# Performance work log

Measured on AMD Instinct MI355X. Metric: run time of the kernel, lower is better.

Reference implementation:

```python
import jax, jax.numpy as jnp
import numpy as np

B, S, I, C, P = 64, 14, 32, 10, 4   # batch, spatial, in-caps/pos, classes, pose size
ROUTINGS = 3
EPS = 1e-9


def setup_inputs() -> dict:
    key = jax.random.key(0)
    k1, k2, k3, k4, k5 = jax.random.split(key, 5)
    return {
        "inputs_pose": jax.random.normal(k1, (B, S, S, I, P, P), jnp.float32),
        "inputs_activation": jax.random.uniform(k2, (B, S, S, I), jnp.float32),
        "w": jax.random.normal(k3, (1, I, C, P, P), jnp.float32),
        "beta_v": jax.random.normal(k4, (1, C), jnp.float32) * 0.1,
        "beta_a": jax.random.normal(k5, (1, C), jnp.float32) * 0.1,
    }


def _em_routing(votes, i_act, beta_v, beta_a, routings):
    # votes: [B, N, C, 16], i_act: [B, N]
    Bn, N, Cc, D = votes.shape
    rr = jnp.full((Bn, N, Cc, 1), 1.0 / Cc, votes.dtype)  # uniform init assignments
    bv = beta_v.reshape(1, 1, Cc, 1)
    ba = beta_a.reshape(1, 1, Cc, 1)
    it_min, it_max = 1.0, min(float(routings), 3.0)  # inverse-temperature schedule
    o_mean = o_act = None
    for it in range(routings):
        inv_temp = it_min + (it_max - it_min) * it / max(1.0, routings - 1.0)
        # --- M step ---
        rr_p = rr * i_act[:, :, None, None]                        # [B,N,C,1]
        rr_sum = jnp.sum(rr_p, axis=1, keepdims=True)              # [B,1,C,1]
        o_mean = jnp.sum(rr_p * votes, axis=1, keepdims=True) / rr_sum   # [B,1,C,16]
        o_var = jnp.sum(rr_p * jnp.square(votes - o_mean), axis=1, keepdims=True) / rr_sum
        o_stdv = jnp.sqrt(o_var)                                   # [B,1,C,16]
        cost = jnp.sum((bv + jnp.log(o_stdv + EPS)) * rr_sum, axis=-1, keepdims=True)  # [B,1,C,1]
        o_act = jax.nn.sigmoid(inv_temp * (ba - cost))             # [B,1,C,1]
        # --- E step (skipped on last iteration) ---
        if it < routings - 1:
            logp = (-jnp.sum(jnp.square(votes - o_mean) / (2.0 * jnp.square(o_stdv) + EPS),
                             axis=-1, keepdims=True)
                    - jnp.sum(jnp.log(o_stdv + EPS), axis=-1, keepdims=True))  # [B,N,C,1]
            zz = jnp.log(o_act + EPS) + logp
            rr = jax.nn.softmax(zz, axis=2)
    return o_mean[:, 0], o_act[:, 0, :, 0]  # [B,C,16], [B,C]


def reference(inputs_pose, inputs_activation, w, beta_v, beta_a):
    # mat_transform: votes[b,h,w,i,c] = pose[b,h,w,i] @ W[i,c]   (4x4 matmuls)
    votes = jnp.einsum('bhwipq,icqr->bhwicpr', inputs_pose, w[0])
    votes = votes.reshape(B, S, S, I, C, P * P)
    # coordinate addition: scaled (row+0.5)/S onto pose element 0, col onto element 1
    coord = (jnp.arange(S, dtype=votes.dtype) + 0.5) / S
    votes = votes.at[..., 0].add(coord[None, :, None, None, None])
    votes = votes.at[..., 1].add(coord[None, None, :, None, None])
    votes = votes.reshape(B, S * S * I, C, P * P)
    acts = inputs_activation.reshape(B, S * S * I)
    o_mean, o_act = _em_routing(votes, acts, beta_v, beta_a, ROUTINGS)
    pose = o_mean.reshape(B, C, P, P)
    return pose, o_act
```

## Files before the change

### kernel.cpp

```cpp
#include <hip/hip_runtime.h>
#include <math.h>

#define Bsz 64
#define Ssz 14
#define Isz 32
#define Csz 10
#define Dsz 16
#define Nsz (Ssz*Ssz*Isz)
#define EPSF 1e-9f

#define CH  640
#define NCH 10

__device__ __forceinline__ void load_pose(const float* __restrict__ poseb, int n, float* p)
{
    const float4* pp = reinterpret_cast<const float4*>(poseb + (size_t)n * Dsz);
    float4 a0 = pp[0], a1 = pp[1], a2 = pp[2], a3 = pp[3];
    p[0]=a0.x; p[1]=a0.y; p[2]=a0.z; p[3]=a0.w;
    p[4]=a1.x; p[5]=a1.y; p[6]=a1.z; p[7]=a1.w;
    p[8]=a2.x; p[9]=a2.y; p[10]=a2.z; p[11]=a2.w;
    p[12]=a3.x; p[13]=a3.y; p[14]=a3.z; p[15]=a3.w;
}

__device__ __forceinline__ void vote_reg(const float* p, const float* Wr,
                                         float chh, float cww, float* v)
{
#pragma unroll
    for (int pr = 0; pr < 4; ++pr)
#pragma unroll
        for (int r = 0; r < 4; ++r)
            v[pr*4+r] = p[pr*4+0]*Wr[0*4+r] + p[pr*4+1]*Wr[1*4+r]
                      + p[pr*4+2]*Wr[2*4+r] + p[pr*4+3]*Wr[3*4+r];
    v[0] += chh;
    v[1] += cww;
}

__device__ __forceinline__ void load_W_regs(const float* __restrict__ w,
                                            int lane, int c, float* Wr)
{
    const float4* ws = reinterpret_cast<const float4*>(w + (((lane & 31)*Csz + c) * Dsz));
    float4 b0 = ws[0], b1 = ws[1], b2 = ws[2], b3 = ws[3];
    Wr[0]=b0.x; Wr[1]=b0.y; Wr[2]=b0.z; Wr[3]=b0.w;
    Wr[4]=b1.x; Wr[5]=b1.y; Wr[6]=b1.z; Wr[7]=b1.w;
    Wr[8]=b2.x; Wr[9]=b2.y; Wr[10]=b2.z; Wr[11]=b2.w;
    Wr[12]=b3.x; Wr[13]=b3.y; Wr[14]=b3.z; Wr[15]=b3.w;
}

__global__ __launch_bounds__(640) void m0_kernel(
    const float* __restrict__ pose,
    const float* __restrict__ act,
    const float* __restrict__ w,
    float* __restrict__ partials)
{
    const int b = blockIdx.x, chunk = blockIdx.y;
    const int tid = threadIdx.x, c = tid >> 6, lane = tid & 63;

    float Wr[16];
    load_W_regs(w, lane, c, Wr);

    float s0 = 0.f, s1[Dsz], s2[Dsz];
#pragma unroll
    for (int d = 0; d < Dsz; ++d) { s1[d] = 0.f; s2[d] = 0.f; }

    const float* poseb = pose + (size_t)b * Nsz * Dsz;
    const float* actb  = act  + (size_t)b * Nsz;
    const int base = chunk * CH;

    for (int nl = lane; nl < CH; nl += 64) {
        const int n = base + nl;
        if (n < Nsz) {
            float p[16];
            load_pose(poseb, n, p);
            int hw = n >> 5;
            int wc = hw % Ssz, hr = hw / Ssz;
            float wgt = actb[n] * (1.0f/Csz);
            float v[16];
            vote_reg(p, Wr, (hr+0.5f)*(1.0f/Ssz), (wc+0.5f)*(1.0f/Ssz), v);
            s0 += wgt;
#pragma unroll
            for (int d = 0; d < Dsz; ++d) {
                float wv = wgt * v[d];
                s1[d] += wv;
                s2[d] += wv * v[d];
            }
        }
    }

#pragma unroll
    for (int m = 32; m >= 1; m >>= 1) {
        s0 += __shfl_xor(s0, m);
#pragma unroll
        for (int d = 0; d < Dsz; ++d) {
            s1[d] += __shfl_xor(s1[d], m);
            s2[d] += __shfl_xor(s2[d], m);
        }
    }
    if (lane == 0) {
        float* pt = partials + ((size_t)(b*Csz + c)*NCH + chunk)*33;
        pt[0] = s0;
#pragma unroll
        for (int d = 0; d < Dsz; ++d) { pt[1+d] = s1[d]; pt[17+d] = s2[d]; }
    }
}

__global__ __launch_bounds__(640) void em_kernel(
    const float* __restrict__ pose,
    const float* __restrict__ act,
    const float* __restrict__ w,
    const float* __restrict__ beta_v,
    const float* __restrict__ beta_a,
    const float* __restrict__ part_in,
    float* __restrict__ part_out,
    float inv_temp_prev)
{
    const int b = blockIdx.x, chunk = blockIdx.y;
    const int tid = threadIdx.x, wv = tid >> 6, lane = tid & 63;

    __shared__ float zz[CH][11];
    __shared__ float Sv[Csz][33];
    __shared__ float prm[Csz][33];
    __shared__ float lg[Csz][16];

    float Wr[16];
    load_W_regs(w, lane, wv, Wr);

    if (tid < Csz*33) {
        int c = tid / 33, j = tid - c*33;
        const float* pp = part_in + ((size_t)(b*Csz + c)*NCH)*33 + j;
        float s = 0.f;
        for (int ch2 = 0; ch2 < NCH; ++ch2) s += pp[ch2*33];
        Sv[c][j] = s;
    }
    __syncthreads();
    if (tid < Csz*Dsz) {
        int c = tid >> 4, d = tid & 15;
        float S0 = Sv[c][0];
        float mn  = Sv[c][1+d] / S0;
        float var = fmaxf(Sv[c][17+d] / S0 - mn*mn, 0.f);
        prm[c][d]    = mn;
        prm[c][16+d] = 1.f / (2.f*var + EPSF);
        lg[c][d]     = __logf(sqrtf(var) + EPSF);
    }
    __syncthreads();
    if (tid < Csz) {
        int c = tid;
        float sumlog = 0.f;
#pragma unroll
        for (int d = 0; d < Dsz; ++d) sumlog += lg[c][d];
        float cost = Sv[c][0] * (16.f * beta_v[c] + sumlog);
        float oact = 1.f / (1.f + __expf(-inv_temp_prev * (beta_a[c] - cost)));
        prm[c][32] = __logf(oact + EPSF) - sumlog;
    }
    __syncthreads();

    const int base = chunk * CH;
    const float* poseb = pose + (size_t)b * Nsz * Dsz;

    {
        float mn[Dsz], iv[Dsz];
#pragma unroll
        for (int d = 0; d < Dsz; ++d) { mn[d] = prm[wv][d]; iv[d] = prm[wv][16+d]; }
        float Kc = prm[wv][32];

        for (int nl = lane; nl < CH; nl += 64) {
            const int n = base + nl;
            if (n < Nsz) {
                float p[16];
                load_pose(poseb, n, p);
                int hw = n >> 5;
                int wc = hw % Ssz, hr = hw / Ssz;
                float v[16];
                vote_reg(p, Wr, (hr+0.5f)*(1.0f/Ssz), (wc+0.5f)*(1.0f/Ssz), v);
                float quad = 0.f;
#pragma unroll
                for (int d = 0; d < Dsz; ++d) {
                    float dv = v[d] - mn[d];
                    quad += dv * dv * iv[d];
                }
                zz[nl][wv] = Kc - quad;
            }
        }
    }
    __syncthreads();

    {
        const int n = base + tid;
        if (n < Nsz) {
            float z[Csz];
#pragma unroll
            for (int c = 0; c < Csz; ++c) z[c] = zz[tid][c];
            float zmax = z[0];
#pragma unroll
            for (int c = 1; c < Csz; ++c) zmax = fmaxf(zmax, z[c]);
            float zsum = 0.f;
#pragma unroll
            for (int c = 0; c < Csz; ++c) { z[c] = __expf(z[c] - zmax); zsum += z[c]; }
            float sc = __fdividef(act[(size_t)b*Nsz + n], zsum);
#pragma unroll
            for (int c = 0; c < Csz; ++c) zz[tid][c] = z[c] * sc;
        }
    }
    __syncthreads();

    float s0 = 0.f, s1[Dsz], s2[Dsz];
#pragma unroll
    for (int d = 0; d < Dsz; ++d) { s1[d] = 0.f; s2[d] = 0.f; }

    for (int nl = lane; nl < CH; nl += 64) {
        const int n = base + nl;
        if (n < Nsz) {
            float p[16];
            load_pose(poseb, n, p);
            int hw = n >> 5;
            int wc = hw % Ssz, hr = hw / Ssz;
            float wgt = zz[nl][wv];
            float v[16];
            vote_reg(p, Wr, (hr+0.5f)*(1.0f/Ssz), (wc+0.5f)*(1.0f/Ssz), v);
            s0 += wgt;
#pragma unroll
            for (int d = 0; d < Dsz; ++d) {
                float wvv = wgt * v[d];
                s1[d] += wvv;
                s2[d] += wvv * v[d];
            }
        }
    }

#pragma unroll
    for (int m = 32; m >= 1; m >>= 1) {
        s0 += __shfl_xor(s0, m);
#pragma unroll
        for (int d = 0; d < Dsz; ++d) {
            s1[d] += __shfl_xor(s1[d], m);
            s2[d] += __shfl_xor(s2[d], m);
        }
    }
    if (lane == 0) {
        float* pt = part_out + ((size_t)(b*Csz + wv)*NCH + chunk)*33;
        pt[0] = s0;
#pragma unroll
        for (int d = 0; d < Dsz; ++d) { pt[1+d] = s1[d]; pt[17+d] = s2[d]; }
    }
}

__global__ __launch_bounds__(64) void fin_kernel(
    const float* __restrict__ partials,
    const float* __restrict__ beta_v,
    const float* __restrict__ beta_a,
    float* __restrict__ out,
    float inv_temp)
{
    const int bc = blockIdx.x * 64 + threadIdx.x;
    if (bc >= Bsz*Csz) return;
    const int c = bc % Csz;

    float S[33];
#pragma unroll
    for (int j = 0; j < 33; ++j) S[j] = 0.f;
    const float* pb = partials + (size_t)bc * NCH * 33;
    for (int ch2 = 0; ch2 < NCH; ++ch2)
#pragma unroll
        for (int j = 0; j < 33; ++j) S[j] += pb[ch2*33 + j];

    float S0 = S[0], rS0 = 1.f / S0;
    float sumlog = 0.f;
    float* om = out + (size_t)bc * Dsz;
#pragma unroll
    for (int d = 0; d < Dsz; ++d) {
        float mn  = S[1+d] * rS0;
        float var = fmaxf(S[17+d] * rS0 - mn*mn, 0.f);
        sumlog += __logf(sqrtf(var) + EPSF);
        om[d] = mn;
    }
    float cost = S0 * (16.f * beta_v[c] + sumlog);
    float oact = 1.f / (1.f + __expf(-inv_temp * (beta_a[c] - cost)));
    out[Bsz*Csz*Dsz + bc] = oact;
}

extern "C" void kernel_launch(void* const* d_in, const int* in_sizes, int n_in,
                              void* d_out, int out_size, void* d_ws, size_t ws_size,
                              hipStream_t stream)
{
    const float* pose = (const float*)d_in[0];
    const float* act  = (const float*)d_in[1];
    const float* w    = (const float*)d_in[2];
    const float* bv   = (const float*)d_in[3];
    const float* ba   = (const float*)d_in[4];
    float* out = (float*)d_out;

    float* partA = (float*)d_ws;
    float* partB = partA + (size_t)Bsz*Csz*NCH*33;

    dim3 grid(Bsz, NCH);

    m0_kernel<<<grid, CH, 0, stream>>>(pose, act, w, partA);
    em_kernel<<<grid, CH, 0, stream>>>(pose, act, w, bv, ba, partA, partB, 1.0f);
    em_kernel<<<grid, CH, 0, stream>>>(pose, act, w, bv, ba, partB, partA, 2.0f);
    fin_kernel<<<(Bsz*Csz + 63)/64, 64, 0, stream>>>(partA, bv, ba, out, 3.0f);
}
```

Baseline: 233.2 us.

## Stage pose chunk in LDS and rechunk N into exact 448-element tiles

Each block now copies its chunk of pose matrices into shared memory once, cooperatively with float4 loads. The ten class wavefronts then read that chunk from LDS instead of each re-reading it from global memory. The chunk size changes from 640 to 448 so that the 6272 inputs split evenly into 14 chunks; this removes the bounds checks and the partially empty last chunk, while the block stays at 640 threads. The cost is about 28 KB more shared memory per block, which may reduce occupancy, and the 64-byte per-lane stride of the LDS reads can cause bank conflicts.

```diff
diff --git a/kernel.cpp b/kernel.cpp
--- a/kernel.cpp
+++ b/kernel.cpp
@@ -9,18 +9,10 @@
 #define Nsz (Ssz*Ssz*Isz)
 #define EPSF 1e-9f
 
-#define CH  640
-#define NCH 10
-
-__device__ __forceinline__ void load_pose(const float* __restrict__ poseb, int n, float* p)
-{
-    const float4* pp = reinterpret_cast<const float4*>(poseb + (size_t)n * Dsz);
-    float4 a0 = pp[0], a1 = pp[1], a2 = pp[2], a3 = pp[3];
-    p[0]=a0.x; p[1]=a0.y; p[2]=a0.z; p[3]=a0.w;
-    p[4]=a1.x; p[5]=a1.y; p[6]=a1.z; p[7]=a1.w;
-    p[8]=a2.x; p[9]=a2.y; p[10]=a2.z; p[11]=a2.w;
-    p[12]=a3.x; p[13]=a3.y; p[14]=a3.z; p[15]=a3.w;
-}
+#define CH   448
+#define NCH  14
+#define BLK  640
+#define ITER (CH/64)
 
 __device__ __forceinline__ void vote_reg(const float* p, const float* Wr,
                                          float chh, float cww, float* v)
@@ -46,7 +38,17 @@
     Wr[12]=b3.x; Wr[13]=b3.y; Wr[14]=b3.z; Wr[15]=b3.w;
 }
 
-__global__ __launch_bounds__(640) void m0_kernel(
+__device__ __forceinline__ void load_pose_lds(const float* Pl, int nl, float* p)
+{
+    const float4* pp = reinterpret_cast<const float4*>(Pl + nl*Dsz);
+    float4 a0 = pp[0], a1 = pp[1], a2 = pp[2], a3 = pp[3];
+    p[0]=a0.x; p[1]=a0.y; p[2]=a0.z; p[3]=a0.w;
+    p[4]=a1.x; p[5]=a1.y; p[6]=a1.z; p[7]=a1.w;
+    p[8]=a2.x; p[9]=a2.y; p[10]=a2.z; p[11]=a2.w;
+    p[12]=a3.x; p[13]=a3.y; p[14]=a3.z; p[15]=a3.w;
+}
+
+__global__ __launch_bounds__(BLK) void m0_kernel(
     const float* __restrict__ pose,
     const float* __restrict__ act,
     const float* __restrict__ w,
@@ -54,35 +56,43 @@
 {
     const int b = blockIdx.x, chunk = blockIdx.y;
     const int tid = threadIdx.x, c = tid >> 6, lane = tid & 63;
+    const int base = chunk * CH;
+
+    __shared__ float Pl[CH*Dsz];
+
+    const float* poseb = pose + (size_t)b * Nsz * Dsz;
+    {
+        const float4* gp = reinterpret_cast<const float4*>(poseb + (size_t)base * Dsz);
+        float4* lp = reinterpret_cast<float4*>(Pl);
+        for (int t = tid; t < CH*4; t += BLK) lp[t] = gp[t];
+    }
 
     float Wr[16];
     load_W_regs(w, lane, c, Wr);
+    __syncthreads();
 
     float s0 = 0.f, s1[Dsz], s2[Dsz];
 #pragma unroll
     for (int d = 0; d < Dsz; ++d) { s1[d] = 0.f; s2[d] = 0.f; }
 
-    const float* poseb = pose + (size_t)b * Nsz * Dsz;
-    const float* actb  = act  + (size_t)b * Nsz;
-    const int base = chunk * CH;
-
-    for (int nl = lane; nl < CH; nl += 64) {
-        const int n = base + nl;
-        if (n < Nsz) {
-            float p[16];
-            load_pose(poseb, n, p);
-            int hw = n >> 5;
-            int wc = hw % Ssz, hr = hw / Ssz;
-            float wgt = actb[n] * (1.0f/Csz);
-            float v[16];
-            vote_reg(p, Wr, (hr+0.5f)*(1.0f/Ssz), (wc+0.5f)*(1.0f/Ssz), v);
-            s0 += wgt;
-#pragma unroll
-            for (int d = 0; d < Dsz; ++d) {
-                float wv = wgt * v[d];
-                s1[d] += wv;
-                s2[d] += wv * v[d];
-            }
+    const float* actb = act + (size_t)b * Nsz;
+
+    for (int it = 0; it < ITER; ++it) {
+        const int nl = it*64 + lane;
+        const int n  = base + nl;
+        float p[16];
+        load_pose_lds(Pl, nl, p);
+        int hw = n >> 5;
+        int wc = hw % Ssz, hr = hw / Ssz;
+        float wgt = actb[n] * (1.0f/Csz);
+        float v[16];
+        vote_reg(p, Wr, (hr+0.5f)*(1.0f/Ssz), (wc+0.5f)*(1.0f/Ssz), v);
+        s0 += wgt;
+#pragma unroll
+        for (int d = 0; d < Dsz; ++d) {
+            float wv = wgt * v[d];
+            s1[d] += wv;
+            s2[d] += wv * v[d];
         }
     }
 
@@ -103,7 +113,7 @@
     }
 }
 
-__global__ __launch_bounds__(640) void em_kernel(
+__global__ __launch_bounds__(BLK) void em_kernel(
     const float* __restrict__ pose,
     const float* __restrict__ act,
     const float* __restrict__ w,
@@ -115,11 +125,20 @@
 {
     const int b = blockIdx.x, chunk = blockIdx.y;
     const int tid = threadIdx.x, wv = tid >> 6, lane = tid & 63;
-
+    const int base = chunk * CH;
+
+    __shared__ float Pl[CH*Dsz];
     __shared__ float zz[CH][11];
     __shared__ float Sv[Csz][33];
     __shared__ float prm[Csz][33];
     __shared__ float lg[Csz][16];
+
+    const float* poseb = pose + (size_t)b * Nsz * Dsz;
+    {
+        const float4* gp = reinterpret_cast<const float4*>(poseb + (size_t)base * Dsz);
+        float4* lp = reinterpret_cast<float4*>(Pl);
+        for (int t = tid; t < CH*4; t += BLK) lp[t] = gp[t];
+    }
 
     float Wr[16];
     load_W_regs(w, lane, wv, Wr);
@@ -153,76 +172,69 @@
     }
     __syncthreads();
 
-    const int base = chunk * CH;
-    const float* poseb = pose + (size_t)b * Nsz * Dsz;
-
     {
         float mn[Dsz], iv[Dsz];
 #pragma unroll
         for (int d = 0; d < Dsz; ++d) { mn[d] = prm[wv][d]; iv[d] = prm[wv][16+d]; }
         float Kc = prm[wv][32];
 
-        for (int nl = lane; nl < CH; nl += 64) {
-            const int n = base + nl;
-            if (n < Nsz) {
-                float p[16];
-                load_pose(poseb, n, p);
-                int hw = n >> 5;
-                int wc = hw % Ssz, hr = hw / Ssz;
-                float v[16];
-                vote_reg(p, Wr, (hr+0.5f)*(1.0f/Ssz), (wc+0.5f)*(1.0f/Ssz), v);
-                float quad = 0.f;
-#pragma unroll
-                for (int d = 0; d < Dsz; ++d) {
-                    float dv = v[d] - mn[d];
-                    quad += dv * dv * iv[d];
-                }
-                zz[nl][wv] = Kc - quad;
-            }
-        }
-    }
-    __syncthreads();
-
-    {
-        const int n = base + tid;
-        if (n < Nsz) {
-            float z[Csz];
-#pragma unroll
-            for (int c = 0; c < Csz; ++c) z[c] = zz[tid][c];
-            float zmax = z[0];
-#pragma unroll
-            for (int c = 1; c < Csz; ++c) zmax = fmaxf(zmax, z[c]);
-            float zsum = 0.f;
-#pragma unroll
-            for (int c = 0; c < Csz; ++c) { z[c] = __expf(z[c] - zmax); zsum += z[c]; }
-            float sc = __fdividef(act[(size_t)b*Nsz + n], zsum);
-#pragma unroll
-            for (int c = 0; c < Csz; ++c) zz[tid][c] = z[c] * sc;
-        }
-    }
-    __syncthreads();
-
-    float s0 = 0.f, s1[Dsz], s2[Dsz];
-#pragma unroll
-    for (int d = 0; d < Dsz; ++d) { s1[d] = 0.f; s2[d] = 0.f; }
-
-    for (int nl = lane; nl < CH; nl += 64) {
-        const int n = base + nl;
-        if (n < Nsz) {
+        for (int it = 0; it < ITER; ++it) {
+            const int nl = it*64 + lane;
+            const int n  = base + nl;
             float p[16];
-            load_pose(poseb, n, p);
+            load_pose_lds(Pl, nl, p);
             int hw = n >> 5;
             int wc = hw % Ssz, hr = hw / Ssz;
-            float wgt = zz[nl][wv];
             float v[16];
             vote_reg(p, Wr, (hr+0.5f)*(1.0f/Ssz), (wc+0.5f)*(1.0f/Ssz), v);
-            s0 += wgt;
+            float quad = 0.f;
 #pragma unroll
             for (int d = 0; d < Dsz; ++d) {
-                float wvv = wgt * v[d];
-                s1[d] += wvv;
-                s2[d] += wvv * v[d];
+                float dv = v[d] - mn[d];
+                quad += dv * dv * iv[d];
             }
+            zz[nl][wv] = Kc - quad;
+        }
+    }
+    __syncthreads();
+
+    if (tid < CH) {
+        const int n = base + tid;
+        float z[Csz];
+#pragma unroll
+        for (int c = 0; c < Csz; ++c) z[c] = zz[tid][c];
+        float zmax = z[0];
+#pragma unroll
+        for (int c = 1; c < Csz; ++c) zmax = fmaxf(zmax, z[c]);
+        float zsum = 0.f;
+#pragma unroll
+        for (int c = 0; c < Csz; ++c) { z[c] = __expf(z[c] - zmax); zsum += z[c]; }
+        float sc = __fdividef(act[(size_t)b*Nsz + n], zsum);
+#pragma unroll
+        for (int c = 0; c < Csz; ++c) zz[tid][c] = z[c] * sc;
+    }
+    __syncthreads();
+
+    float s0 = 0.f, s1[Dsz], s2[Dsz];
+#pragma unroll
+    for (int d = 0; d < Dsz; ++d) { s1[d] = 0.f; s2[d] = 0.f; }
+
+    for (int it = 0; it < ITER; ++it) {
+        const int nl = it*64 + lane;
+        const int n  = base + nl;
+        float p[16];
+        load_pose_lds(Pl, nl, p);
+        int hw = n >> 5;
+        int wc = hw % Ssz, hr = hw / Ssz;
+        float wgt = zz[nl][wv];
+        float v[16];
+        vote_reg(p, Wr, (hr+0.5f)*(1.0f/Ssz), (wc+0.5f)*(1.0f/Ssz), v);
+        s0 += wgt;
+#pragma unroll
+        for (int d = 0; d < Dsz; ++d) {
+            float wvv = wgt * v[d];
+            s1[d] += wvv;
+            s2[d] += wvv * v[d];
         }
     }
 
@@ -293,8 +305,8 @@
 
     dim3 grid(Bsz, NCH);
 
-    m0_kernel<<<grid, CH, 0, stream>>>(pose, act, w, partA);
-    em_kernel<<<grid, CH, 0, stream>>>(pose, act, w, bv, ba, partA, partB, 1.0f);
-    em_kernel<<<grid, CH, 0, stream>>>(pose, act, w, bv, ba, partB, partA, 2.0f);
+    m0_kernel<<<grid, BLK, 0, stream>>>(pose, act, w, partA);
+    em_kernel<<<grid, BLK, 0, stream>>>(pose, act, w, bv, ba, partA, partB, 1.0f);
+    em_kernel<<<grid, BLK, 0, stream>>>(pose, act, w, bv, ba, partB, partA, 2.0f);
     fin_kernel<<<(Bsz*Csz + 63)/64, 64, 0, stream>>>(partA, bv, ba, out, 3.0f);
 }
```

After: 238.8 us. 2.4% more time.
